# Performance work log

Hardware: AMD Instinct MI355X
Metric: run time of the kernel (lower is better)

The kernel has to match this reference:

```python
import jax, jax.numpy as jnp
import numpy as np

CHANNELS_CHOICE = np.array([8, 16, 24, 32, 40, 48, 56, 64])
MAX_C = 64
B, H, W_SP = 128, 32, 32
N_EDGES = 6
# edge list per intermediate node: (edge_weight_index, source_node_index)
EDGES = [[(0, 0)], [(1, 0), (2, 1)], [(3, 0), (4, 1), (5, 2)]]


def setup_inputs() -> dict:
    key = jax.random.key(0)
    k1, k2, k3, k4 = jax.random.split(key, 4)
    inputs = jax.random.normal(k1, (B, MAX_C, H, W_SP), dtype=jnp.float32)
    alphas1 = jax.random.uniform(k2, (8,), dtype=jnp.float32)  # input-width arch weights
    alphas2 = jax.random.uniform(k3, (8,), dtype=jnp.float32)  # output-width arch weights
    # shared master 3x3 conv weight per edge (OIHW)
    W = jax.random.normal(k4, (N_EDGES, MAX_C, MAX_C, 3, 3), dtype=jnp.float32) * 0.05
    return {"inputs": inputs, "alphas1": alphas1, "alphas2": alphas2, "W": W}


def _channel_scale(alphas1, alphas2, dtype):
    # mask[c, i] = 1 if channel c is inside width choice CHANNELS_CHOICE[i]
    mask = (jnp.arange(MAX_C)[:, None] < jnp.asarray(CHANNELS_CHOICE)[None, :]).astype(dtype)  # [64, 8]
    a_in = mask @ alphas1   # [64] cumulative input-channel weight
    a_out = mask @ alphas2  # [64] cumulative output-channel weight
    return a_out[:, None] * a_in[None, :]  # [64, 64]


def _edge(x, w, scale):
    # weighted-combi of all (c1, c2) channel-sliced sub-convs == one conv with scaled weight
    w_eff = w * scale[:, :, None, None]
    return jax.lax.conv_general_dilated(
        jax.nn.relu(x), w_eff, window_strides=(1, 1), padding="SAME",
        dimension_numbers=("NCHW", "OIHW", "NCHW"))


def reference(inputs, alphas1, alphas2, W):
    scale = _channel_scale(alphas1, alphas2, inputs.dtype)
    nodes = [inputs]
    for node_edges in EDGES:
        feat = 0.0
        for l, src in node_edges:
            feat = feat + _edge(nodes[src], W[l], scale)
        nodes.append(feat)
    return nodes[-1]
```

## Files before the change

kernel.cpp:

```cpp
#include <hip/hip_runtime.h>
#include <hip/hip_bf16.h>


typedef __bf16 bf16x8 __attribute__((ext_vector_type(8)));
typedef float floatx4 __attribute__((ext_vector_type(4)));
typedef unsigned int uint32;
typedef uint32 u32x4 __attribute__((ext_vector_type(4)));

#define PADW 34
#define PIMG (PADW * PADW)
#define ROWB (PADW * 64 * 2)
#define A_LDS (18 * ROWB)
#define A_CHUNKS (A_LDS / 16)
#define A_TAIL (A_CHUNKS - 9 * 512)
#define TAPB (64 * 64 * 2)
#define B_LDS (9 * TAPB)
#define SMEM_BYTES (A_LDS + B_LDS)

__device__ __forceinline__ void gld16(const char* g, char* l) {
    __builtin_amdgcn_global_load_lds(
        (const __attribute__((address_space(1))) uint32*)g,
        (__attribute__((address_space(3))) uint32*)l, 16, 0, 0);
}

__global__ __launch_bounds__(256) void pre_kernel(
    const float* __restrict__ in, const float* __restrict__ a1,
    const float* __restrict__ a2, const float* __restrict__ W,
    __hip_bfloat16* __restrict__ wt, __hip_bfloat16* __restrict__ wtR,
    __hip_bfloat16* __restrict__ r0, __hip_bfloat16* __restrict__ r1,
    __hip_bfloat16* __restrict__ r2) {
    __shared__ float tile[32][65];
    int blk = blockIdx.x;
    int tid = threadIdx.x;

    if (blk < 864) {
        int idx = blk * 256 + tid;
        int i = idx & 63;
        int o = (idx >> 6) & 63;
        int rest = idx >> 12;
        int t = rest % 9;
        int l = rest / 9;
        int ji = i >> 3, jo = o >> 3;
        float ain = 0.f, aout = 0.f;
#pragma unroll
        for (int j = 0; j < 8; ++j) {
            ain  += (j >= ji) ? a1[j] : 0.f;
            aout += (j >= jo) ? a2[j] : 0.f;
        }
        float v = W[(size_t)((l * 64 + o) * 64 + i) * 9 + t] * ain * aout;
        int os = ((o & 3) << 4) + (o >> 2);
        size_t e = (size_t)(l * 9 + t) * 4096 + os * 64 +
                   ((((i >> 3) ^ (os & 7)) << 3) + (i & 7));
        __hip_bfloat16 bv = __float2bfloat16(v);
        wt[e] = bv;
        int n  = os >> 4, c15 = os & 15;
        int q  = i >> 5, quad = (i >> 3) & 3, ee = i & 7;
        int ln = (quad << 4) + c15;
        size_t e2 = (size_t)(l * 9 + t) * 4096 + (((q << 2) + n) << 9) +
                    (ln << 3) + ee;
        wtR[e2] = bv;
    } else if (blk < 992) {
        int b = blk - 864;
        __hip_bfloat16* bufs[3] = {r0, r1, r2};
#pragma unroll
        for (int f = 0; f < 3; ++f) {
            uint32* buf = (uint32*)(bufs[f] + (size_t)b * PIMG * 64);
            for (int idx = tid; idx < 132 * 32; idx += 256) {
                int slot = idx >> 5, u = idx & 31;
                int yy, xx;
                if (slot < 34)      { yy = 0;  xx = slot; }
                else if (slot < 68) { yy = 33; xx = slot - 34; }
                else { int s2 = slot - 68; yy = 1 + (s2 >> 1); xx = (s2 & 1) * 33; }
                buf[(size_t)(yy * PADW + xx) * 32 + u] = 0u;
            }
        }
    } else {
        int rb = blk - 992;
        int b = rb >> 5, y = rb & 31;
        int x = tid & 31, c0 = tid >> 5;
        const float* ip = in + ((size_t)b * 64 * 32 + y) * 32 + x;
#pragma unroll
        for (int cc = 0; cc < 8; ++cc) {
            int c = cc * 8 + c0;
            tile[x][c] = fmaxf(ip[(size_t)c * 1024], 0.f);
        }
        __syncthreads();
        int j = tid & 7, xq = tid >> 3;
        int p = (b * PADW + y + 1) * PADW + 1 + xq;
        alignas(16) __hip_bfloat16 hv[8];
#pragma unroll
        for (int k = 0; k < 8; ++k)
            hv[k] = __float2bfloat16(tile[xq][j * 8 + k]);
        *(uint4*)((char*)r0 + (size_t)p * 128 + ((j ^ (p & 7)) << 4)) =
            *(const uint4*)hv;
    }
}

#define ZERO4(A_)                                                        \
    _Pragma("unroll") for (int m_ = 0; m_ < 4; ++m_)                     \
    _Pragma("unroll") for (int n_ = 0; n_ < 4; ++n_)                     \
        A_[m_][n_] = (floatx4){0.f, 0.f, 0.f, 0.f};

template <int MODE>
__global__ __launch_bounds__(512, 1) void conv_k(
    const __hip_bfloat16* __restrict__ Asrc,
    const __hip_bfloat16* __restrict__ wt,
    const __hip_bfloat16* __restrict__ wtR,
    __hip_bfloat16* __restrict__ nodeOut, float* __restrict__ finalOut,
    __hip_bfloat16* __restrict__ p2, __hip_bfloat16* __restrict__ p3) {
    extern __shared__ char smem[];
    char* smemB = smem + A_LDS;
    int tid = threadIdx.x;
    int wv = tid >> 6, lane = tid & 63;
    int quad = lane >> 4, l15 = lane & 15;
    int blk = blockIdx.x;
    int b = blk >> 1, y0 = (blk & 1) << 4;
    const size_t aOff = (size_t)(b * PADW + y0) * PADW * 128;
    const size_t pbase = ((size_t)blk * 512 + tid) << 7;

    auto stage_A = [&]() {
        const char* gA = (const char*)Asrc + aOff;
#pragma unroll
        for (int it = 0; it < 10; ++it) {
            int c = it * 512 + tid;
            if (it < 9 || tid < A_TAIL)
                gld16(gA + (size_t)c * 16, smem + (it * 512 + wv * 64) * 16);
        }
    };
    auto stage_B = [&](int l) {
        const char* gB = (const char*)wt + (size_t)l * 9 * TAPB;
#pragma unroll
        for (int it = 0; it < 9; ++it) {
            int c = it * 512 + tid;
            gld16(gB + (size_t)c * 16, smemB + (it * 512 + wv * 64) * 16);
        }
    };
    auto ldA = [&](int tl, int q, bf16x8 (&dst)[4]) {
        const int ky = tl / 3, kx = tl % 3;
#pragma unroll
        for (int m = 0; m < 4; ++m) {
            int arow = 2 * wv + (m >> 1) + ky;
            int apx  = ((m & 1) << 4) + l15 + kx;
            int R = b * PADW + y0 + arow;
            int slot = ((q << 2) + quad) ^ ((2 * R + apx) & 7);
            dst[m] = *(const bf16x8*)(smem + arow * ROWB + apx * 128 +
                                      slot * 16);
        }
    };
    auto ldB = [&](int tl, int q, bf16x8 (&dst)[4]) {
#pragma unroll
        for (int n = 0; n < 4; ++n) {
            int o = (n << 4) + l15;
            int slot = ((q << 2) + quad) ^ (l15 & 7);
            dst[n] = *(const bf16x8*)(smemB + tl * TAPB + o * 128 +
                                      slot * 16);
        }
    };
    auto init_p = [&](floatx4 (&acc)[4][4], const __hip_bfloat16* p) {
#pragma unroll
        for (int c = 0; c < 8; ++c) {
            alignas(16) __hip_bfloat16 hv[8];
            *(uint4*)hv = *(const uint4*)((const char*)p + pbase + c * 16);
#pragma unroll
            for (int k = 0; k < 8; ++k) {
                int j = c * 8 + k;
                acc[j >> 4][(j >> 2) & 3][j & 3] = __bfloat162float(hv[k]);
            }
        }
    };
    auto epi_p = [&](floatx4 (&acc)[4][4], __hip_bfloat16* p) {
#pragma unroll
        for (int c = 0; c < 8; ++c) {
            alignas(16) __hip_bfloat16 hv[8];
#pragma unroll
            for (int k = 0; k < 8; ++k) {
                int j = c * 8 + k;
                hv[k] = __float2bfloat16(acc[j >> 4][(j >> 2) & 3][j & 3]);
            }
            *(uint4*)((char*)p + pbase + c * 16) = *(const uint4*)hv;
        }
    };
    auto epi_node = [&](floatx4 (&acc)[4][4], __hip_bfloat16* dst) {
#pragma unroll
        for (int m = 0; m < 4; ++m) {
            int row = y0 + 2 * wv + (m >> 1);
#pragma unroll
            for (int r = 0; r < 4; ++r) {
                int x = ((m & 1) << 4) + (quad << 2) + r;
                int p = (b * PADW + row + 1) * PADW + x + 1;
                alignas(8) __hip_bfloat16 hv[4];
#pragma unroll
                for (int n = 0; n < 4; ++n)
                    hv[n] = __float2bfloat16(fmaxf(acc[m][n][r], 0.f));
                char* d8 = (char*)dst + (size_t)p * 128 +
                           ((((l15 >> 1) ^ (p & 7)) << 4) + ((l15 & 1) << 3));
                *(uint2*)d8 = *(const uint2*)hv;
            }
        }
    };
    auto paired_pass = [&](int lR, floatx4 (&accL)[4][4],
                           floatx4 (&accR)[4][4]) {
        const char* gR = (const char*)wtR + (size_t)lR * 9 * TAPB;
#pragma unroll
        for (int t = 0; t < 9; ++t) {
            u32x4 Bb[8];
#pragma unroll
            for (int f = 0; f < 8; ++f)
                Bb[f] = *(const __attribute__((address_space(1))) u32x4*)
                    (gR + (size_t)t * TAPB + (f << 10) + (lane << 4));
#pragma unroll
            for (int q = 0; q < 2; ++q) {
                bf16x8 Af[4], Bf[4];
                ldA(t, q, Af);
                ldB(t, q, Bf);
                __builtin_amdgcn_s_setprio(1);
#pragma unroll
                for (int m = 0; m < 4; ++m)
#pragma unroll
                    for (int n = 0; n < 4; ++n)
                        accL[m][n] = __builtin_amdgcn_mfma_f32_16x16x32_bf16(
                            Af[m], Bf[n], accL[m][n], 0, 0, 0);
#pragma unroll
                for (int n = 0; n < 4; ++n) {
                    bf16x8 Br = __builtin_bit_cast(bf16x8, Bb[(q << 2) + n]);
#pragma unroll
                    for (int m = 0; m < 4; ++m)
                        accR[m][n] = __builtin_amdgcn_mfma_f32_16x16x32_bf16(
                            Af[m], Br, accR[m][n], 0, 0, 0);
                }
                __builtin_amdgcn_s_setprio(0);
            }
        }
    };
    auto single_pass = [&](floatx4 (&acc)[4][4]) {
        bf16x8 fA[2][4], fB[2][4];
        ldA(0, 0, fA[0]);
        ldB(0, 0, fB[0]);
#pragma unroll
        for (int st = 0; st < 18; ++st) {
            const int pb = st & 1;
            if (st < 17) {
                const int nt = (st + 1) >> 1, nq = (st + 1) & 1;
                ldA(nt, nq, fA[pb ^ 1]);
                ldB(nt, nq, fB[pb ^ 1]);
            }
            __builtin_amdgcn_s_setprio(1);
#pragma unroll
            for (int m = 0; m < 4; ++m)
#pragma unroll
                for (int n = 0; n < 4; ++n)
                    acc[m][n] = __builtin_amdgcn_mfma_f32_16x16x32_bf16(
                        fA[pb][m], fB[pb][n], acc[m][n], 0, 0, 0);
            __builtin_amdgcn_s_setprio(0);
        }
    };

    if constexpr (MODE == 1) {
        stage_A();
        stage_B(0);
        floatx4 aT[4][4], aX[4][4];
        ZERO4(aT); ZERO4(aX);
        __syncthreads();
        paired_pass(1, aT, aX);
        epi_node(aT, nodeOut);
        epi_p(aX, p2);
        __syncthreads();
        stage_B(3);
        __syncthreads();
        floatx4 aY[4][4];
        ZERO4(aY);
        single_pass(aY);
        epi_p(aY, p3);
    } else if constexpr (MODE == 2) {
        stage_A();
        stage_B(2);
        floatx4 aX[4][4], aY[4][4];
        init_p(aX, p2);
        init_p(aY, p3);
        __syncthreads();
        paired_pass(4, aX, aY);
        epi_node(aX, nodeOut);
        epi_p(aY, p3);
    } else {
        stage_A();
        stage_B(5);
        floatx4 aY[4][4];
        init_p(aY, p3);
        __syncthreads();
        single_pass(aY);
#pragma unroll
        for (int m = 0; m < 4; ++m) {
            int row = y0 + 2 * wv + (m >> 1);
#pragma unroll
            for (int n = 0; n < 4; ++n) {
                int o = (l15 << 2) + n;
                *(floatx4*)(finalOut +
                            (((size_t)b * 64 + o) * 32 + row) * 32 +
                            ((m & 1) << 4) + (quad << 2)) = aY[m][n];
            }
        }
    }
}

extern "C" void kernel_launch(void* const* d_in, const int* in_sizes, int n_in,
                              void* d_out, int out_size, void* d_ws,
                              size_t ws_size, hipStream_t stream) {
    const float* inputs  = (const float*)d_in[0];
    const float* alphas1 = (const float*)d_in[1];
    const float* alphas2 = (const float*)d_in[2];
    const float* W       = (const float*)d_in[3];
    char* ws = (char*)d_ws;

    __hip_bfloat16* wt  = (__hip_bfloat16*)(ws);
    __hip_bfloat16* wtR = (__hip_bfloat16*)(ws + ((size_t)1 << 19));
    __hip_bfloat16* r0 = (__hip_bfloat16*)(ws + ((size_t)1 << 20));
    __hip_bfloat16* r1 = (__hip_bfloat16*)(ws + ((size_t)20 << 20));
    __hip_bfloat16* r2 = (__hip_bfloat16*)(ws + ((size_t)40 << 20));
    __hip_bfloat16* p2 = (__hip_bfloat16*)(ws + ((size_t)60 << 20));
    __hip_bfloat16* p3 = (__hip_bfloat16*)(ws + ((size_t)80 << 20));
    float* out = (float*)d_out;

    (void)hipFuncSetAttribute((const void*)conv_k<1>,
                              hipFuncAttributeMaxDynamicSharedMemorySize,
                              SMEM_BYTES);
    (void)hipFuncSetAttribute((const void*)conv_k<2>,
                              hipFuncAttributeMaxDynamicSharedMemorySize,
                              SMEM_BYTES);
    (void)hipFuncSetAttribute((const void*)conv_k<3>,
                              hipFuncAttributeMaxDynamicSharedMemorySize,
                              SMEM_BYTES);

    pre_kernel<<<864 + 128 + 4096, 256, 0, stream>>>(
        inputs, alphas1, alphas2, W, wt, wtR, r0, r1, r2);
    conv_k<1><<<256, 512, SMEM_BYTES, stream>>>(r0, wt, wtR, r1, nullptr,
                                                p2, p3);
    conv_k<2><<<256, 512, SMEM_BYTES, stream>>>(r1, wt, wtR, r2, nullptr,
                                                p2, p3);
    conv_k<3><<<256, 512, SMEM_BYTES, stream>>>(r2, wt, wtR, nullptr, out,
                                                p2, p3);
}
```

Before: 176.6 us.

## Split conv tiles to 8 rows per 256-thread block and prefetch global weights

Each conv block now covers 8 output rows with 256 threads instead of 16 rows with 512 threads, so the grid doubles to 512 blocks and the input tile in LDS shrinks to 10 padded rows. The paired pass is restructured into a double-buffered 18-step loop that prefetches the next LDS fragments and the next tap's global weight registers while the current MFMAs run, hiding load latency. The barrier is moved before the accumulator init. The tradeoffs are more halo rows reloaded in total, each block restaging the full weight set, and higher register pressure from the doubled buffers.

```diff
diff --git a/kernel.cpp b/kernel.cpp
--- a/kernel.cpp
+++ b/kernel.cpp
@@ -10,9 +10,9 @@
 #define PADW 34
 #define PIMG (PADW * PADW)
 #define ROWB (PADW * 64 * 2)
-#define A_LDS (18 * ROWB)
+#define A_LDS (10 * ROWB)
 #define A_CHUNKS (A_LDS / 16)
-#define A_TAIL (A_CHUNKS - 9 * 512)
+#define A_TAIL (A_CHUNKS - 10 * 256)
 #define TAPB (64 * 64 * 2)
 #define B_LDS (9 * TAPB)
 #define SMEM_BYTES (A_LDS + B_LDS)
@@ -102,7 +102,7 @@
         A_[m_][n_] = (floatx4){0.f, 0.f, 0.f, 0.f};
 
 template <int MODE>
-__global__ __launch_bounds__(512, 1) void conv_k(
+__global__ __launch_bounds__(256, 1) void conv_k(
     const __hip_bfloat16* __restrict__ Asrc,
     const __hip_bfloat16* __restrict__ wt,
     const __hip_bfloat16* __restrict__ wtR,
@@ -114,25 +114,26 @@
     int wv = tid >> 6, lane = tid & 63;
     int quad = lane >> 4, l15 = lane & 15;
     int blk = blockIdx.x;
-    int b = blk >> 1, y0 = (blk & 1) << 4;
-    const size_t aOff = (size_t)(b * PADW + y0) * PADW * 128;
-    const size_t pbase = ((size_t)blk * 512 + tid) << 7;
+    int b = blk >> 2, y0 = (blk & 3) << 3;
+    const int Rb = b * PADW + y0;
+    const size_t aOff = (size_t)Rb * PADW * 128;
+    const size_t pbase = ((size_t)blk * 256 + tid) << 7;
 
     auto stage_A = [&]() {
         const char* gA = (const char*)Asrc + aOff;
 #pragma unroll
-        for (int it = 0; it < 10; ++it) {
-            int c = it * 512 + tid;
-            if (it < 9 || tid < A_TAIL)
-                gld16(gA + (size_t)c * 16, smem + (it * 512 + wv * 64) * 16);
+        for (int it = 0; it < 11; ++it) {
+            int c = it * 256 + tid;
+            if (it < 10 || tid < A_TAIL)
+                gld16(gA + (size_t)c * 16, smem + (it * 256 + wv * 64) * 16);
         }
     };
     auto stage_B = [&](int l) {
         const char* gB = (const char*)wt + (size_t)l * 9 * TAPB;
 #pragma unroll
-        for (int it = 0; it < 9; ++it) {
-            int c = it * 512 + tid;
-            gld16(gB + (size_t)c * 16, smemB + (it * 512 + wv * 64) * 16);
+        for (int it = 0; it < 18; ++it) {
+            int c = it * 256 + tid;
+            gld16(gB + (size_t)c * 16, smemB + (it * 256 + wv * 64) * 16);
         }
     };
     auto ldA = [&](int tl, int q, bf16x8 (&dst)[4]) {
@@ -141,7 +142,7 @@
         for (int m = 0; m < 4; ++m) {
             int arow = 2 * wv + (m >> 1) + ky;
             int apx  = ((m & 1) << 4) + l15 + kx;
-            int R = b * PADW + y0 + arow;
+            int R = Rb + arow;
             int slot = ((q << 2) + quad) ^ ((2 * R + apx) & 7);
             dst[m] = *(const bf16x8*)(smem + arow * ROWB + apx * 128 +
                                       slot * 16);
@@ -201,35 +202,43 @@
     auto paired_pass = [&](int lR, floatx4 (&accL)[4][4],
                            floatx4 (&accR)[4][4]) {
         const char* gR = (const char*)wtR + (size_t)lR * 9 * TAPB;
-#pragma unroll
-        for (int t = 0; t < 9; ++t) {
-            u32x4 Bb[8];
+        auto ldBg = [&](int t, u32x4 (&dst)[8]) {
 #pragma unroll
             for (int f = 0; f < 8; ++f)
-                Bb[f] = *(const __attribute__((address_space(1))) u32x4*)
+                dst[f] = *(const __attribute__((address_space(1))) u32x4*)
                     (gR + (size_t)t * TAPB + (f << 10) + (lane << 4));
-#pragma unroll
-            for (int q = 0; q < 2; ++q) {
-                bf16x8 Af[4], Bf[4];
-                ldA(t, q, Af);
-                ldB(t, q, Bf);
-                __builtin_amdgcn_s_setprio(1);
+        };
+        bf16x8 Af[2][4], Bf[2][4];
+        u32x4 Bb[2][8];
+        ldBg(0, Bb[0]);
+        ldA(0, 0, Af[0]);
+        ldB(0, 0, Bf[0]);
+#pragma unroll
+        for (int st = 0; st < 18; ++st) {
+            const int pb = st & 1, t = st >> 1;
+            if (st < 17) {
+                const int nt = (st + 1) >> 1, nq = (st + 1) & 1;
+                ldA(nt, nq, Af[pb ^ 1]);
+                ldB(nt, nq, Bf[pb ^ 1]);
+            }
+            if (pb == 0 && t < 8) ldBg(t + 1, Bb[(t + 1) & 1]);
+            __builtin_amdgcn_s_setprio(1);
+#pragma unroll
+            for (int m = 0; m < 4; ++m)
+#pragma unroll
+                for (int n = 0; n < 4; ++n)
+                    accL[m][n] = __builtin_amdgcn_mfma_f32_16x16x32_bf16(
+                        Af[pb][m], Bf[pb][n], accL[m][n], 0, 0, 0);
+#pragma unroll
+            for (int n = 0; n < 4; ++n) {
+                bf16x8 Br = __builtin_bit_cast(bf16x8,
+                                               Bb[t & 1][(pb << 2) + n]);
 #pragma unroll
                 for (int m = 0; m < 4; ++m)
-#pragma unroll
-                    for (int n = 0; n < 4; ++n)
-                        accL[m][n] = __builtin_amdgcn_mfma_f32_16x16x32_bf16(
-                            Af[m], Bf[n], accL[m][n], 0, 0, 0);
-#pragma unroll
-                for (int n = 0; n < 4; ++n) {
-                    bf16x8 Br = __builtin_bit_cast(bf16x8, Bb[(q << 2) + n]);
-#pragma unroll
-                    for (int m = 0; m < 4; ++m)
-                        accR[m][n] = __builtin_amdgcn_mfma_f32_16x16x32_bf16(
-                            Af[m], Br, accR[m][n], 0, 0, 0);
-                }
-                __builtin_amdgcn_s_setprio(0);
-            }
+                    accR[m][n] = __builtin_amdgcn_mfma_f32_16x16x32_bf16(
+                        Af[pb][m], Br, accR[m][n], 0, 0, 0);
+            }
+            __builtin_amdgcn_s_setprio(0);
         }
     };
     auto single_pass = [&](floatx4 (&acc)[4][4]) {
@@ -250,7 +259,7 @@
 #pragma unroll
                 for (int n = 0; n < 4; ++n)
                     acc[m][n] = __builtin_amdgcn_mfma_f32_16x16x32_bf16(
-                        fA[pb][m], fB[pb][n], acc[m][n], 0, 0, 0);
+                        fA[pb][m], fB[pb][n], acc[pb ? m : m][n], 0, 0, 0);
             __builtin_amdgcn_s_setprio(0);
         }
     };
@@ -258,9 +267,9 @@
     if constexpr (MODE == 1) {
         stage_A();
         stage_B(0);
+        __syncthreads();
         floatx4 aT[4][4], aX[4][4];
         ZERO4(aT); ZERO4(aX);
-        __syncthreads();
         paired_pass(1, aT, aX);
         epi_node(aT, nodeOut);
         epi_p(aX, p2);
@@ -274,19 +283,19 @@
     } else if constexpr (MODE == 2) {
         stage_A();
         stage_B(2);
+        __syncthreads();
         floatx4 aX[4][4], aY[4][4];
         init_p(aX, p2);
         init_p(aY, p3);
-        __syncthreads();
         paired_pass(4, aX, aY);
         epi_node(aX, nodeOut);
         epi_p(aY, p3);
     } else {
         stage_A();
         stage_B(5);
+        __syncthreads();
         floatx4 aY[4][4];
         init_p(aY, p3);
-        __syncthreads();
         single_pass(aY);
 #pragma unroll
         for (int m = 0; m < 4; ++m) {
@@ -332,10 +341,10 @@
 
     pre_kernel<<<864 + 128 + 4096, 256, 0, stream>>>(
         inputs, alphas1, alphas2, W, wt, wtR, r0, r1, r2);
-    conv_k<1><<<256, 512, SMEM_BYTES, stream>>>(r0, wt, wtR, r1, nullptr,
+    conv_k<1><<<512, 256, SMEM_BYTES, stream>>>(r0, wt, wtR, r1, nullptr,
                                                 p2, p3);
-    conv_k<2><<<256, 512, SMEM_BYTES, stream>>>(r1, wt, wtR, r2, nullptr,
+    conv_k<2><<<512, 256, SMEM_BYTES, stream>>>(r1, wt, wtR, r2, nullptr,
                                                 p2, p3);
-    conv_k<3><<<256, 512, SMEM_BYTES, stream>>>(r2, wt, wtR, nullptr, out,
+    conv_k<3><<<512, 256, SMEM_BYTES, stream>>>(r2, wt, wtR, nullptr, out,
                                                 p2, p3);
 }
```

New measurement: 180.0 us. About the same (+1.9%).
